# Kernel optimization log

Hardware: AMD Instinct MI355X
Metric: run time of the kernel (lower is better)

The kernel has to match this reference:

```python
import jax, jax.numpy as jnp
import numpy as np
from jax.scipy.special import erfc

# ---- static config (matches init_kwargs) ----
N_ATOMS = 16384
NUM_BATCH = 32
N_PAIRS = 1_048_576
KMAX = 8
CUTOFF = 10.0
ON_CUT = 0.25 * CUTOFF   # 2.5
OFF_CUT = 0.75 * CUTOFF  # 7.5
ALPHA = 4.0 / CUTOFF + 0.001
ALPHA2 = ALPHA * ALPHA
TWO_PI = 2.0 * np.pi
ONE_OVER_SQRTPI = 1.0 / np.sqrt(np.pi)
EPS = 1e-8


def _make_kmul():
    r = np.arange(-KMAX, KMAX + 1)
    kx, ky, kz = np.meshgrid(r, r, r, indexing='ij')
    k = np.stack([kx, ky, kz], axis=-1).reshape(-1, 3).astype(np.float32)
    k2 = np.sum(k * k, axis=-1)
    k = k[(k2 > 0) & (k2 <= KMAX ** 2)]  # exclude k=0, spherical cutoff
    return k  # [K, 3]


def setup_inputs() -> dict:
    key = jax.random.key(0)
    ks = jax.random.split(key, 6)
    Qa = 0.5 * jax.random.normal(ks[0], (N_ATOMS,), dtype=jnp.float32)
    rij = 0.5 + 9.5 * jax.random.uniform(ks[1], (N_PAIRS,), dtype=jnp.float32)
    R = 20.0 * jax.random.uniform(ks[2], (N_ATOMS, 3), dtype=jnp.float32)
    boxlen = 18.0 + 4.0 * jax.random.uniform(ks[3], (NUM_BATCH, 3), dtype=jnp.float32)
    cell = boxlen[:, :, None] * jnp.eye(3, dtype=jnp.float32)[None]  # diagonal boxes [B,3,3]
    idx_i = jnp.sort(jax.random.randint(ks[4], (N_PAIRS,), 0, N_ATOMS)).astype(jnp.int32)
    idx_j = jax.random.randint(ks[5], (N_PAIRS,), 0, N_ATOMS).astype(jnp.int32)
    batch_seg = jnp.repeat(jnp.arange(NUM_BATCH, dtype=jnp.int32), N_ATOMS // NUM_BATCH)
    kmul = jnp.asarray(_make_kmul())
    return {"Qa": Qa, "rij": rij, "R": R, "cell": cell, "kmul": kmul,
            "idx_i": idx_i, "idx_j": idx_j, "batch_seg": batch_seg}


def _switch_component(x):
    x_safe = jnp.where(x <= 0, jnp.ones_like(x), x)
    return jnp.where(x <= 0, jnp.zeros_like(x), jnp.exp(-1.0 / x_safe))


def _switch_function(r):
    # smooth C-inf switch: 1 for r<=ON_CUT, 0 for r>=OFF_CUT
    x = (r - ON_CUT) / (OFF_CUT - ON_CUT)
    fp = _switch_component(x)
    fm = _switch_component(1.0 - x)
    return jnp.where(x <= 0, jnp.ones_like(x),
                     jnp.where(x >= 1, jnp.zeros_like(x), fm / (fp + fm)))


def _real_space(Qa, rij, idx_i, idx_j):
    fac = Qa[idx_i] * Qa[idx_j]                    # gather per pair
    f = _switch_function(rij)
    coulomb = 1.0 / rij
    damped = 1.0 / jnp.sqrt(rij * rij + 1.0)
    pw = fac * (f * damped + (1.0 - f) * coulomb) * erfc(ALPHA * rij)
    return jax.ops.segment_sum(pw, idx_i, num_segments=N_ATOMS)  # [N]


def _reciprocal_space(q, R, cell, kmul, batch_seg):
    box_length = jnp.diagonal(cell, axis1=-2, axis2=-1)            # [B,3]
    k = TWO_PI * kmul[None, :, :] / box_length[:, None, :]         # [B,K,3]
    k2 = jnp.sum(k * k, axis=-1)                                   # [B,K]
    qg = jnp.exp(-0.25 * k2 / ALPHA2) / k2                         # [B,K]
    dot = jnp.sum(k[batch_seg] * R[:, None, :], axis=-1)           # [N,K]
    qcos = q[:, None] * jnp.cos(dot)                               # [N,K]
    qsin = q[:, None] * jnp.sin(dot)
    q_real = jax.ops.segment_sum(qcos, batch_seg, num_segments=NUM_BATCH)  # [B,K]
    q_imag = jax.ops.segment_sum(qsin, batch_seg, num_segments=NUM_BATCH)
    qf = q_real * q_real + q_imag * q_imag
    e_recip_b = TWO_PI / jnp.prod(box_length, axis=1) * jnp.sum(qf * qg, axis=-1)  # [B]
    q2 = q * q
    e_self = ALPHA * ONE_OVER_SQRTPI * q2                          # [N]
    w = q2 + EPS
    wnorm = jax.ops.segment_sum(w, batch_seg, num_segments=NUM_BATCH)
    w = w / wnorm[batch_seg]
    return w * e_recip_b[batch_seg] - e_self                       # [N]


def reference(Qa, rij, R, cell, kmul, idx_i, idx_j, batch_seg):
    e_real = _real_space(Qa, rij, idx_i, idx_j)
    e_recip = _reciprocal_space(Qa, R, cell, kmul, batch_seg)
    return e_real + e_recip  # per-atom electrostatic energy [N]
```

## Files before the change

### kernel.cpp

```cpp
#include <hip/hip_runtime.h>

#define N_ATOMS 16384
#define NUM_BATCH 32
#define N_PAIRS 1048576
#define ATOMS_PER_BATCH 512

#define C_TWO_PI 6.28318530717958647692f
#define C_ALPHA 0.401f
#define C_ALPHA2 0.160801f
#define C_SELF 0.22624002f
#define C_EPS 1e-8f

__device__ __forceinline__ float switch_fn(float r) {
    float x = (r - 2.5f) * 0.2f;
    if (x <= 0.0f) return 1.0f;
    if (x >= 1.0f) return 0.0f;
    float fp = __expf(-1.0f / x);
    float fm = __expf(-1.0f / (1.0f - x));
    return fm / (fp + fm);
}

#define ASPLIT 4

__global__ __launch_bounds__(256) void recip_kernel(
    const float* __restrict__ Qa, const float* __restrict__ R,
    const float* __restrict__ cell, const float* __restrict__ kmul,
    float* __restrict__ partials, int K, int nchunk) {
    __shared__ float4 at[ATOMS_PER_BATCH];
    __shared__ float pr[ASPLIT][64];
    __shared__ float pi_[ASPLIT][64];

    int b  = blockIdx.y;
    int tx = threadIdx.x;
    int ty = threadIdx.y;
    int flat = ty * 64 + tx;

    float Lx = cell[b * 9 + 0], Ly = cell[b * 9 + 4], Lz = cell[b * 9 + 8];
    float iLx = 1.0f / Lx, iLy = 1.0f / Ly, iLz = 1.0f / Lz;

    int abase = b * ATOMS_PER_BATCH;
    for (int a = flat; a < ATOMS_PER_BATCH; a += 256) {
        int n = abase + a;
        at[a] = make_float4(R[3 * n + 0] * iLx, R[3 * n + 1] * iLy,
                            R[3 * n + 2] * iLz, Qa[n]);
    }
    __syncthreads();

    int K2 = K >> 1;
    int kk = K2 + blockIdx.x * 64 + tx;
    bool valid = kk < K;
    int kki = valid ? kk : K2;
    float mx = kmul[3 * kki + 0];
    float my = kmul[3 * kki + 1];
    float mz = kmul[3 * kki + 2];

    float cr = 0.0f, ci = 0.0f;
    int a0 = ty * (ATOMS_PER_BATCH / ASPLIT);
#pragma unroll 4
    for (int a = a0; a < a0 + (ATOMS_PER_BATCH / ASPLIT); ++a) {
        float4 v = at[a];
        float dr = mx * v.x + my * v.y + mz * v.z;
        float ang = C_TWO_PI * (dr - rintf(dr));
        cr = fmaf(v.w, __cosf(ang), cr);
        ci = fmaf(v.w, __sinf(ang), ci);
    }

    if (ty > 0) { pr[ty][tx] = cr; pi_[ty][tx] = ci; }
    __syncthreads();
    if (ty == 0) {
#pragma unroll
        for (int s = 1; s < ASPLIT; ++s) { cr += pr[s][tx]; ci += pi_[s][tx]; }
        float kx = C_TWO_PI * mx * iLx;
        float ky = C_TWO_PI * my * iLy;
        float kz = C_TWO_PI * mz * iLz;
        float k2 = kx * kx + ky * ky + kz * kz;
        float qg = __expf(-0.25f * k2 / C_ALPHA2) / k2;
        float contrib = valid ? 2.0f * (cr * cr + ci * ci) * qg : 0.0f;
#pragma unroll
        for (int off = 32; off > 0; off >>= 1)
            contrib += __shfl_down(contrib, off);
        if (tx == 0)
            partials[b * nchunk + blockIdx.x] =
                (C_TWO_PI / (Lx * Ly * Lz)) * contrib;
    }
}

__device__ __forceinline__ int lower_bound64(const int* __restrict__ arr, int key) {
    int lane = threadIdx.x & 63;
    int lo = 0, size = N_PAIRS;
    while (size > 64) {
        int chunk = (size + 63) >> 6;
        int pos = lo + (lane + 1) * chunk;
        int v = (pos < lo + size) ? arr[pos] : 0x7fffffff;
        unsigned long long m = __ballot(v < key);
        int cnt = __popcll(m);
        int nlo = lo + cnt * chunk;
        size = min(chunk, lo + size - nlo);
        lo = nlo;
    }
    int pos = lo + lane;
    int v = (lane < size) ? arr[pos] : 0x7fffffff;
    unsigned long long m = __ballot(v < key);
    return lo + __popcll(m);
}

#define SUBS 16
#define NA (ATOMS_PER_BATCH / SUBS)

__global__ __launch_bounds__(256) void final_kernel(
    const float* __restrict__ Qa, const float* __restrict__ rij,
    const int* __restrict__ idx_i, const int* __restrict__ idx_j,
    const float* __restrict__ partials, int nchunk,
    float* __restrict__ out) {
    __shared__ float accs[NA];
    __shared__ float red[4];
    __shared__ float er_s;
    __shared__ int   se[2];

    int b    = blockIdx.x >> 4;
    int sub  = blockIdx.x & 15;
    int tid  = threadIdx.x;
    int wave = tid >> 6;
    int abase = b * ATOMS_PER_BATCH;
    int A0 = abase + sub * NA;

    if (tid < NA) accs[tid] = 0.0f;

    float q0 = Qa[abase + tid];
    float q1 = Qa[abase + 256 + tid];
    float s = fmaf(q0, q0, C_EPS) + fmaf(q1, q1, C_EPS);
#pragma unroll
    for (int off = 32; off > 0; off >>= 1) s += __shfl_down(s, off);
    if ((tid & 63) == 0) red[wave] = s;

    if (wave == 0) {
        int r = lower_bound64(idx_i, A0);
        if ((tid & 63) == 0) se[0] = r;
    } else if (wave == 1) {
        int r = lower_bound64(idx_i, A0 + NA);
        if ((tid & 63) == 0) se[1] = r;
    } else if (wave == 2) {
        int c = tid - 128;
        float er = (c < nchunk) ? partials[b * nchunk + c] : 0.0f;
#pragma unroll
        for (int off = 32; off > 0; off >>= 1) er += __shfl_down(er, off);
        if (c == 0) er_s = er;
    }
    __syncthreads();

    float wnorm   = red[0] + red[1] + red[2] + red[3];
    float e_recip = er_s;
    int start = se[0], end = se[1];

    int s4 = start >> 2;
    int e4 = (end + 3) >> 2;
    for (int g4 = s4 + tid; g4 < e4; g4 += 256) {
        int4   ii = ((const int4*)idx_i)[g4];
        int4   jj = ((const int4*)idx_j)[g4];
        float4 rr = ((const float4*)rij)[g4];
        int   is[4] = {ii.x, ii.y, ii.z, ii.w};
        int   js[4] = {jj.x, jj.y, jj.z, jj.w};
        float rs[4] = {rr.x, rr.y, rr.z, rr.w};
        int cur = -1;
        float acc = 0.0f;
        int p0 = g4 << 2;
#pragma unroll
        for (int u = 0; u < 4; ++u) {
            int p = p0 + u;
            if (p < start || p >= end) continue;
            float r = rs[u];
            float f = switch_fn(r);
            float coul   = __builtin_amdgcn_rcpf(r);
            float damped = __builtin_amdgcn_rsqf(fmaf(r, r, 1.0f));
            float pw = Qa[is[u]] * Qa[js[u]] *
                       (f * damped + (1.0f - f) * coul) * erfcf(C_ALPHA * r);
            if (is[u] != cur) {
                if (cur >= 0) atomicAdd(&accs[cur - A0], acc);
                cur = is[u];
                acc = 0.0f;
            }
            acc += pw;
        }
        if (cur >= 0) atomicAdd(&accs[cur - A0], acc);
    }
    __syncthreads();

    if (tid < NA) {
        int atom = A0 + tid;
        float q = Qa[atom];
        float q2 = q * q;
        float w = (q2 + C_EPS) / wnorm;
        out[atom] = accs[tid] + w * e_recip - C_SELF * q2;
    }
}

extern "C" void kernel_launch(void* const* d_in, const int* in_sizes, int n_in,
                              void* d_out, int out_size, void* d_ws, size_t ws_size,
                              hipStream_t stream) {
    const float* Qa   = (const float*)d_in[0];
    const float* rij  = (const float*)d_in[1];
    const float* R    = (const float*)d_in[2];
    const float* cell = (const float*)d_in[3];
    const float* kmul = (const float*)d_in[4];
    const int* idx_i  = (const int*)d_in[5];
    const int* idx_j  = (const int*)d_in[6];
    float* out = (float*)d_out;

    int K = in_sizes[4] / 3;
    int K2 = K / 2;
    int nchunk = (K2 + 63) / 64;

    float* partials = (float*)d_ws;

    dim3 rblock(64, ASPLIT);
    dim3 rgrid(nchunk, NUM_BATCH);
    recip_kernel<<<rgrid, rblock, 0, stream>>>(Qa, R, cell, kmul, partials, K, nchunk);

    final_kernel<<<NUM_BATCH * SUBS, 256, 0, stream>>>(
        Qa, rij, idx_i, idx_j, partials, nchunk, out);
}
```

Measured before the change: 95.58 us.

## Run reciprocal and real-space work concurrently in one launch, combine after

The reciprocal-space block work and the real-space pair blocks are merged into a single kernel whose block index picks the role, so both phases run side by side instead of the pair phase waiting on the reciprocal kernel. Pair blocks write raw per-atom sums to the output. A small combine kernel then adds the weighted reciprocal energy and the self term per batch. This removes the serialization between the two phases, at the cost of an extra read-modify-write of the output and a small third pass.

```diff
diff --git a/kernel.cpp b/kernel.cpp
--- a/kernel.cpp
+++ b/kernel.cpp
@@ -10,6 +10,10 @@
 #define C_ALPHA2 0.160801f
 #define C_SELF 0.22624002f
 #define C_EPS 1e-8f
+
+#define ASPLIT 4
+#define SUBS 16
+#define NA (ATOMS_PER_BATCH / SUBS)
 
 __device__ __forceinline__ float switch_fn(float r) {
     float x = (r - 2.5f) * 0.2f;
@@ -18,71 +22,6 @@
     float fp = __expf(-1.0f / x);
     float fm = __expf(-1.0f / (1.0f - x));
     return fm / (fp + fm);
-}
-
-#define ASPLIT 4
-
-__global__ __launch_bounds__(256) void recip_kernel(
-    const float* __restrict__ Qa, const float* __restrict__ R,
-    const float* __restrict__ cell, const float* __restrict__ kmul,
-    float* __restrict__ partials, int K, int nchunk) {
-    __shared__ float4 at[ATOMS_PER_BATCH];
-    __shared__ float pr[ASPLIT][64];
-    __shared__ float pi_[ASPLIT][64];
-
-    int b  = blockIdx.y;
-    int tx = threadIdx.x;
-    int ty = threadIdx.y;
-    int flat = ty * 64 + tx;
-
-    float Lx = cell[b * 9 + 0], Ly = cell[b * 9 + 4], Lz = cell[b * 9 + 8];
-    float iLx = 1.0f / Lx, iLy = 1.0f / Ly, iLz = 1.0f / Lz;
-
-    int abase = b * ATOMS_PER_BATCH;
-    for (int a = flat; a < ATOMS_PER_BATCH; a += 256) {
-        int n = abase + a;
-        at[a] = make_float4(R[3 * n + 0] * iLx, R[3 * n + 1] * iLy,
-                            R[3 * n + 2] * iLz, Qa[n]);
-    }
-    __syncthreads();
-
-    int K2 = K >> 1;
-    int kk = K2 + blockIdx.x * 64 + tx;
-    bool valid = kk < K;
-    int kki = valid ? kk : K2;
-    float mx = kmul[3 * kki + 0];
-    float my = kmul[3 * kki + 1];
-    float mz = kmul[3 * kki + 2];
-
-    float cr = 0.0f, ci = 0.0f;
-    int a0 = ty * (ATOMS_PER_BATCH / ASPLIT);
-#pragma unroll 4
-    for (int a = a0; a < a0 + (ATOMS_PER_BATCH / ASPLIT); ++a) {
-        float4 v = at[a];
-        float dr = mx * v.x + my * v.y + mz * v.z;
-        float ang = C_TWO_PI * (dr - rintf(dr));
-        cr = fmaf(v.w, __cosf(ang), cr);
-        ci = fmaf(v.w, __sinf(ang), ci);
-    }
-
-    if (ty > 0) { pr[ty][tx] = cr; pi_[ty][tx] = ci; }
-    __syncthreads();
-    if (ty == 0) {
-#pragma unroll
-        for (int s = 1; s < ASPLIT; ++s) { cr += pr[s][tx]; ci += pi_[s][tx]; }
-        float kx = C_TWO_PI * mx * iLx;
-        float ky = C_TWO_PI * my * iLy;
-        float kz = C_TWO_PI * mz * iLz;
-        float k2 = kx * kx + ky * ky + kz * kz;
-        float qg = __expf(-0.25f * k2 / C_ALPHA2) / k2;
-        float contrib = valid ? 2.0f * (cr * cr + ci * ci) * qg : 0.0f;
-#pragma unroll
-        for (int off = 32; off > 0; off >>= 1)
-            contrib += __shfl_down(contrib, off);
-        if (tx == 0)
-            partials[b * nchunk + blockIdx.x] =
-                (C_TWO_PI / (Lx * Ly * Lz)) * contrib;
-    }
 }
 
 __device__ __forceinline__ int lower_bound64(const int* __restrict__ arr, int key) {
@@ -104,43 +43,153 @@
     return lo + __popcll(m);
 }
 
-#define SUBS 16
-#define NA (ATOMS_PER_BATCH / SUBS)
-
-__global__ __launch_bounds__(256) void final_kernel(
+__global__ __launch_bounds__(256) void work_kernel(
     const float* __restrict__ Qa, const float* __restrict__ rij,
+    const float* __restrict__ R, const float* __restrict__ cell,
+    const float* __restrict__ kmul,
     const int* __restrict__ idx_i, const int* __restrict__ idx_j,
-    const float* __restrict__ partials, int nchunk,
+    float* __restrict__ partials, int K, int nchunk,
     float* __restrict__ out) {
-    __shared__ float accs[NA];
+    int nrecip = NUM_BATCH * nchunk;
+    int bx = blockIdx.x;
+    int tid = threadIdx.x;
+
+    if (bx < nrecip) {
+        __shared__ float4 at[ATOMS_PER_BATCH];
+        __shared__ float pr[ASPLIT][64];
+        __shared__ float pi_[ASPLIT][64];
+
+        int b     = bx / nchunk;
+        int chunk = bx - b * nchunk;
+        int tx = tid & 63;
+        int ty = tid >> 6;
+
+        float Lx = cell[b * 9 + 0], Ly = cell[b * 9 + 4], Lz = cell[b * 9 + 8];
+        float iLx = 1.0f / Lx, iLy = 1.0f / Ly, iLz = 1.0f / Lz;
+
+        int abase = b * ATOMS_PER_BATCH;
+        for (int a = tid; a < ATOMS_PER_BATCH; a += 256) {
+            int n = abase + a;
+            at[a] = make_float4(R[3 * n + 0] * iLx, R[3 * n + 1] * iLy,
+                                R[3 * n + 2] * iLz, Qa[n]);
+        }
+        __syncthreads();
+
+        int K2 = K >> 1;
+        int kk = K2 + chunk * 64 + tx;
+        bool valid = kk < K;
+        int kki = valid ? kk : K2;
+        float mx = kmul[3 * kki + 0];
+        float my = kmul[3 * kki + 1];
+        float mz = kmul[3 * kki + 2];
+
+        float cr = 0.0f, ci = 0.0f;
+        int a0 = ty * (ATOMS_PER_BATCH / ASPLIT);
+#pragma unroll 4
+        for (int a = a0; a < a0 + (ATOMS_PER_BATCH / ASPLIT); ++a) {
+            float4 v = at[a];
+            float dr = mx * v.x + my * v.y + mz * v.z;
+            float ang = C_TWO_PI * (dr - rintf(dr));
+            cr = fmaf(v.w, __cosf(ang), cr);
+            ci = fmaf(v.w, __sinf(ang), ci);
+        }
+
+        if (ty > 0) { pr[ty][tx] = cr; pi_[ty][tx] = ci; }
+        __syncthreads();
+        if (ty == 0) {
+#pragma unroll
+            for (int s = 1; s < ASPLIT; ++s) { cr += pr[s][tx]; ci += pi_[s][tx]; }
+            float kx = C_TWO_PI * mx * iLx;
+            float ky = C_TWO_PI * my * iLy;
+            float kz = C_TWO_PI * mz * iLz;
+            float k2 = kx * kx + ky * ky + kz * kz;
+            float qg = __expf(-0.25f * k2 / C_ALPHA2) / k2;
+            float contrib = valid ? 2.0f * (cr * cr + ci * ci) * qg : 0.0f;
+#pragma unroll
+            for (int off = 32; off > 0; off >>= 1)
+                contrib += __shfl_down(contrib, off);
+            if (tx == 0)
+                partials[b * nchunk + chunk] =
+                    (C_TWO_PI / (Lx * Ly * Lz)) * contrib;
+        }
+    } else {
+        __shared__ float accs[NA];
+        __shared__ int se[2];
+
+        int rb  = bx - nrecip;
+        int b   = rb >> 4;
+        int sub = rb & 15;
+        int wave = tid >> 6;
+        int A0 = b * ATOMS_PER_BATCH + sub * NA;
+
+        if (tid < NA) accs[tid] = 0.0f;
+
+        if (wave == 0) {
+            int r = lower_bound64(idx_i, A0);
+            if ((tid & 63) == 0) se[0] = r;
+        } else if (wave == 1) {
+            int r = lower_bound64(idx_i, A0 + NA);
+            if ((tid & 63) == 0) se[1] = r;
+        }
+        __syncthreads();
+
+        int start = se[0], end = se[1];
+        int s4 = start >> 2;
+        int e4 = (end + 3) >> 2;
+        for (int g4 = s4 + tid; g4 < e4; g4 += 256) {
+            int4   ii = ((const int4*)idx_i)[g4];
+            int4   jj = ((const int4*)idx_j)[g4];
+            float4 rr = ((const float4*)rij)[g4];
+            int   is[4] = {ii.x, ii.y, ii.z, ii.w};
+            int   js[4] = {jj.x, jj.y, jj.z, jj.w};
+            float rs[4] = {rr.x, rr.y, rr.z, rr.w};
+            int cur = -1;
+            float acc = 0.0f;
+            int p0 = g4 << 2;
+#pragma unroll
+            for (int u = 0; u < 4; ++u) {
+                int p = p0 + u;
+                if (p < start || p >= end) continue;
+                float r = rs[u];
+                float f = switch_fn(r);
+                float coul   = __builtin_amdgcn_rcpf(r);
+                float damped = __builtin_amdgcn_rsqf(fmaf(r, r, 1.0f));
+                float pw = Qa[is[u]] * Qa[js[u]] *
+                           (f * damped + (1.0f - f) * coul) * erfcf(C_ALPHA * r);
+                if (is[u] != cur) {
+                    if (cur >= 0) atomicAdd(&accs[cur - A0], acc);
+                    cur = is[u];
+                    acc = 0.0f;
+                }
+                acc += pw;
+            }
+            if (cur >= 0) atomicAdd(&accs[cur - A0], acc);
+        }
+        __syncthreads();
+
+        if (tid < NA) out[A0 + tid] = accs[tid];
+    }
+}
+
+__global__ __launch_bounds__(256) void combine_kernel(
+    const float* __restrict__ Qa, const float* __restrict__ partials,
+    int nchunk, float* __restrict__ out) {
     __shared__ float red[4];
     __shared__ float er_s;
-    __shared__ int   se[2];
-
-    int b    = blockIdx.x >> 4;
-    int sub  = blockIdx.x & 15;
-    int tid  = threadIdx.x;
-    int wave = tid >> 6;
+
+    int b = blockIdx.x;
+    int tid = threadIdx.x;
     int abase = b * ATOMS_PER_BATCH;
-    int A0 = abase + sub * NA;
-
-    if (tid < NA) accs[tid] = 0.0f;
 
     float q0 = Qa[abase + tid];
     float q1 = Qa[abase + 256 + tid];
     float s = fmaf(q0, q0, C_EPS) + fmaf(q1, q1, C_EPS);
 #pragma unroll
     for (int off = 32; off > 0; off >>= 1) s += __shfl_down(s, off);
-    if ((tid & 63) == 0) red[wave] = s;
-
-    if (wave == 0) {
-        int r = lower_bound64(idx_i, A0);
-        if ((tid & 63) == 0) se[0] = r;
-    } else if (wave == 1) {
-        int r = lower_bound64(idx_i, A0 + NA);
-        if ((tid & 63) == 0) se[1] = r;
-    } else if (wave == 2) {
-        int c = tid - 128;
+    if ((tid & 63) == 0) red[tid >> 6] = s;
+
+    if (tid >= 64 && tid < 128) {
+        int c = tid - 64;
         float er = (c < nchunk) ? partials[b * nchunk + c] : 0.0f;
 #pragma unroll
         for (int off = 32; off > 0; off >>= 1) er += __shfl_down(er, off);
@@ -148,50 +197,13 @@
     }
     __syncthreads();
 
-    float wnorm   = red[0] + red[1] + red[2] + red[3];
+    float wnorm = red[0] + red[1] + red[2] + red[3];
     float e_recip = er_s;
-    int start = se[0], end = se[1];
-
-    int s4 = start >> 2;
-    int e4 = (end + 3) >> 2;
-    for (int g4 = s4 + tid; g4 < e4; g4 += 256) {
-        int4   ii = ((const int4*)idx_i)[g4];
-        int4   jj = ((const int4*)idx_j)[g4];
-        float4 rr = ((const float4*)rij)[g4];
-        int   is[4] = {ii.x, ii.y, ii.z, ii.w};
-        int   js[4] = {jj.x, jj.y, jj.z, jj.w};
-        float rs[4] = {rr.x, rr.y, rr.z, rr.w};
-        int cur = -1;
-        float acc = 0.0f;
-        int p0 = g4 << 2;
-#pragma unroll
-        for (int u = 0; u < 4; ++u) {
-            int p = p0 + u;
-            if (p < start || p >= end) continue;
-            float r = rs[u];
-            float f = switch_fn(r);
-            float coul   = __builtin_amdgcn_rcpf(r);
-            float damped = __builtin_amdgcn_rsqf(fmaf(r, r, 1.0f));
-            float pw = Qa[is[u]] * Qa[js[u]] *
-                       (f * damped + (1.0f - f) * coul) * erfcf(C_ALPHA * r);
-            if (is[u] != cur) {
-                if (cur >= 0) atomicAdd(&accs[cur - A0], acc);
-                cur = is[u];
-                acc = 0.0f;
-            }
-            acc += pw;
-        }
-        if (cur >= 0) atomicAdd(&accs[cur - A0], acc);
-    }
-    __syncthreads();
-
-    if (tid < NA) {
-        int atom = A0 + tid;
-        float q = Qa[atom];
-        float q2 = q * q;
-        float w = (q2 + C_EPS) / wnorm;
-        out[atom] = accs[tid] + w * e_recip - C_SELF * q2;
-    }
+
+    float q20 = q0 * q0;
+    float q21 = q1 * q1;
+    out[abase + tid]       += (q20 + C_EPS) / wnorm * e_recip - C_SELF * q20;
+    out[abase + 256 + tid] += (q21 + C_EPS) / wnorm * e_recip - C_SELF * q21;
 }
 
 extern "C" void kernel_launch(void* const* d_in, const int* in_sizes, int n_in,
@@ -212,10 +224,9 @@
 
     float* partials = (float*)d_ws;
 
-    dim3 rblock(64, ASPLIT);
-    dim3 rgrid(nchunk, NUM_BATCH);
-    recip_kernel<<<rgrid, rblock, 0, stream>>>(Qa, R, cell, kmul, partials, K, nchunk);
-
-    final_kernel<<<NUM_BATCH * SUBS, 256, 0, stream>>>(
-        Qa, rij, idx_i, idx_j, partials, nchunk, out);
-}
+    int nblocks = NUM_BATCH * nchunk + NUM_BATCH * SUBS;
+    work_kernel<<<nblocks, 256, 0, stream>>>(
+        Qa, rij, R, cell, kmul, idx_i, idx_j, partials, K, nchunk, out);
+
+    combine_kernel<<<NUM_BATCH, 256, 0, stream>>>(Qa, partials, nchunk, out);
+}
```

Measured after the change: 92.95 us. 2.8% less time.
